# Performance work log

Hardware: AMD Instinct MI355X
Metric: run time of the kernel (lower is better)

## Reference

```python
import jax, jax.numpy as jnp
import numpy as np

B, C, H, W = 2, 512, 32, 32
HEADS = 8      # attention heads
GROUPS = 8     # offset groups (defaults to heads)
DH = 64        # dim_head
DF = 4         # downsample_factor
OFF_SCALE = 4.0
EPS = 1e-5


def _bn(t, gamma, beta):
    # eval-mode BatchNorm2d with running_mean=0, running_var=1
    s = gamma / jnp.sqrt(1.0 + EPS)
    return t * s[None, :, None, None] + beta[None, :, None, None]


def _gconv1x1(t, w):
    # grouped 1x1 conv (bias-free); w: (GROUPS, out_per_group, in_per_group)
    b, c, h, ww = t.shape
    o = jnp.einsum('bgci,goc->bgoi', t.reshape(b, GROUPS, c // GROUPS, h * ww), w)
    return o.reshape(b, GROUPS * w.shape[1], h, ww)


def _grid_sample(img, grid):
    # F.grid_sample: bilinear, padding_mode='zeros', align_corners=False
    # img: (N,Ci,Hi,Wi); grid: (N,Hg,Wg,2), grid[...,0]=x, grid[...,1]=y in [-1,1]
    N, Ci, Hi, Wi = img.shape
    gx = (grid[..., 0] + 1.0) * (Wi / 2.0) - 0.5
    gy = (grid[..., 1] + 1.0) * (Hi / 2.0) - 0.5
    x0 = jnp.floor(gx)
    y0 = jnp.floor(gy)
    wx = gx - x0
    wy = gy - y0

    def gather(im, ix, iy):
        valid = (ix >= 0) & (ix < Wi) & (iy >= 0) & (iy < Hi)
        ixc = jnp.clip(ix, 0, Wi - 1).astype(jnp.int32)
        iyc = jnp.clip(iy, 0, Hi - 1).astype(jnp.int32)
        return im[:, iyc, ixc] * valid[None].astype(im.dtype)

    def sample_one(im, x0, y0, wx, wy):
        v00 = gather(im, x0, y0)
        v01 = gather(im, x0 + 1, y0)
        v10 = gather(im, x0, y0 + 1)
        v11 = gather(im, x0 + 1, y0 + 1)
        wx = wx[None]
        wy = wy[None]
        return (v00 * (1 - wx) * (1 - wy) + v01 * wx * (1 - wy)
                + v10 * (1 - wx) * wy + v11 * wx * wy)

    return jax.vmap(sample_one)(img, x0, y0, wx, wy)


def _forward(x, bn1_g, bn1_b, bn2_g, bn2_b, qw, kw, vw, out_w, out_b,
             off_dw_w, off_dw_b, off_pw_w,
             cpb_w1, cpb_b1, cpb_w2, cpb_b2, cpb_w3, cpb_b3,
             mlp_w1, mlp_b1, mlp_w2, mlp_b2):
    b = x.shape[0]
    xn = _bn(x, bn1_g, bn1_b)
    # ---- deformable attention ----
    q = _gconv1x1(xn, qw)                                   # (b, 512, H, W)
    qg = q.reshape(b * GROUPS, DH, H, W)
    # to_offsets: depthwise conv k=6, s=4, p=1 -> GELU -> 1x1(64->2) -> tanh * offset_scale
    off = jax.lax.conv_general_dilated(
        qg, off_dw_w, (DF, DF), ((1, 1), (1, 1)),
        dimension_numbers=('NCHW', 'OIHW', 'NCHW'), feature_group_count=DH)
    off = jax.nn.gelu(off + off_dw_b[None, :, None, None], approximate=False)
    off = jnp.tanh(jnp.einsum('bchw,oc->bohw', off, off_pw_w)) * OFF_SCALE   # (b*G, 2, Hd, Wd)
    Hd, Wd = off.shape[-2], off.shape[-1]
    gy, gx = jnp.meshgrid(jnp.arange(Hd, dtype=x.dtype), jnp.arange(Wd, dtype=x.dtype), indexing='ij')
    vx = gx[None] + off[:, 0]
    vy = gy[None] + off[:, 1]
    # normalize_grid (lucidrains): first comp by (Hd-1), second by (Wd-1)
    nx = 2.0 * vx / max(Hd - 1, 1) - 1.0
    ny = 2.0 * vy / max(Wd - 1, 1) - 1.0
    vgrid_scaled = jnp.stack((nx, ny), axis=-1)             # (b*G, Hd, Wd, 2)
    kv = _grid_sample(xn.reshape(b * GROUPS, DH, H, W), vgrid_scaled)
    kv = kv.reshape(b, GROUPS * DH, Hd, Wd)
    k = _gconv1x1(kv, kw)
    v = _gconv1x1(kv, vw)
    scale = DH ** -0.5
    qh = q.reshape(b, HEADS, DH, H * W).transpose(0, 1, 3, 2) * scale    # (b,h,i,d)
    kh = k.reshape(b, HEADS, DH, Hd * Wd).transpose(0, 1, 3, 2)          # (b,h,j,d)
    vh = v.reshape(b, HEADS, DH, Hd * Wd).transpose(0, 1, 3, 2)
    # continuous relative position bias (CPB)
    qgy, qgx = jnp.meshgrid(jnp.arange(H, dtype=x.dtype), jnp.arange(W, dtype=x.dtype), indexing='ij')
    grid_q = jnp.stack((2.0 * qgx / max(H - 1, 1) - 1.0,
                        2.0 * qgy / max(W - 1, 1) - 1.0), axis=-1).reshape(1, H * W, 2)
    grid_kv = vgrid_scaled.reshape(b * GROUPS, Hd * Wd, 2)
    pos = grid_q[:, :, None, :] - grid_kv[:, None, :, :]    # (b*G, i, j, 2)
    bias = jnp.sign(pos) * jnp.log1p(jnp.abs(pos))
    bias = jax.nn.relu(bias @ cpb_w1 + cpb_b1)
    bias = jax.nn.relu(bias @ cpb_w2 + cpb_b2)
    bias = (bias @ cpb_w3 + cpb_b3).reshape(b, GROUPS, H * W, Hd * Wd)   # heads//groups == 1
    sim = jnp.einsum('bhid,bhjd->bhij', qh, kh) + bias
    attn = jax.nn.softmax(sim, axis=-1)
    out = jnp.einsum('bhij,bhjd->bhid', attn, vh)
    out = out.transpose(0, 1, 3, 2).reshape(b, HEADS * DH, H, W)
    out = jnp.einsum('bchw,oc->bohw', out, out_w) + out_b[None, :, None, None]
    x = x + out
    # ---- conv1x1 MLP ----
    xn2 = _bn(x, bn2_g, bn2_b)
    h1 = jax.nn.gelu(jnp.einsum('bchw,oc->bohw', xn2, mlp_w1) + mlp_b1[None, :, None, None],
                     approximate=False)
    return x + jnp.einsum('bchw,oc->bohw', h1, mlp_w2) + mlp_b2[None, :, None, None]


def setup_inputs():
    ks = jax.random.split(jax.random.key(0), 16)
    w = lambda k, shape: jax.random.normal(k, shape, dtype=jnp.float32) * 0.02
    return {
        'x': jax.random.normal(ks[0], (B, C, H, W), dtype=jnp.float32),
        'bn1_g': jnp.ones((C,), jnp.float32),
        'bn1_b': jnp.zeros((C,), jnp.float32),
        'bn2_g': jnp.ones((C,), jnp.float32),
        'bn2_b': jnp.zeros((C,), jnp.float32),
        'qw': w(ks[1], (GROUPS, DH, C // GROUPS)),
        'kw': w(ks[2], (GROUPS, DH, C // GROUPS)),
        'vw': w(ks[3], (GROUPS, DH, C // GROUPS)),
        'out_w': w(ks[4], (C, HEADS * DH)),
        'out_b': jnp.zeros((C,), jnp.float32),
        'off_dw_w': w(ks[5], (DH, 1, 6, 6)),
        'off_dw_b': jnp.zeros((DH,), jnp.float32),
        'off_pw_w': w(ks[6], (2, DH)),
        'cpb_w1': w(ks[7], (2, 128)),
        'cpb_b1': jnp.zeros((128,), jnp.float32),
        'cpb_w2': w(ks[8], (128, 128)),
        'cpb_b2': jnp.zeros((128,), jnp.float32),
        'cpb_w3': w(ks[9], (128, 1)),
        'cpb_b3': jnp.zeros((1,), jnp.float32),
        'mlp_w1': w(ks[10], (4 * C, C)),
        'mlp_b1': jnp.zeros((4 * C,), jnp.float32),
        'mlp_w2': w(ks[11], (C, 4 * C)),
        'mlp_b2': jnp.zeros((C,), jnp.float32),
    }


def reference(x, bn1_g, bn1_b, bn2_g, bn2_b, qw, kw, vw, out_w, out_b,
              off_dw_w, off_dw_b, off_pw_w,
              cpb_w1, cpb_b1, cpb_w2, cpb_b2, cpb_w3, cpb_b3,
              mlp_w1, mlp_b1, mlp_w2, mlp_b2):
    return _forward(x, bn1_g, bn1_b, bn2_g, bn2_b, qw, kw, vw, out_w, out_b,
                    off_dw_w, off_dw_b, off_pw_w,
                    cpb_w1, cpb_b1, cpb_w2, cpb_b2, cpb_w3, cpb_b3,
                    mlp_w1, mlp_b1, mlp_w2, mlp_b2)
```

## Files before the change

### kernel.cpp

```cpp
#include <hip/hip_runtime.h>
#include <hip/hip_bf16.h>
#include <math.h>

#define BB 2
#define CC 512
#define HH 32
#define WW 32
#define HWP 1024
#define GG 8
#define DH 64
#define HD 8
#define WD 8
#define JJ 64
#define BG 16
#define EPS 1e-5f

typedef __attribute__((ext_vector_type(8))) short short8;
typedef __attribute__((ext_vector_type(4))) short s16x4;
typedef __attribute__((ext_vector_type(4))) float f32x4;
typedef __attribute__((ext_vector_type(4))) unsigned short u16x4;
typedef __attribute__((ext_vector_type(4))) unsigned int u32x4;

static __device__ __forceinline__ short f2bf(float x) {
    unsigned u = __builtin_bit_cast(unsigned, x);
    u += 0x7FFFu + ((u >> 16) & 1u);
    return (short)(u >> 16);
}

__global__ void k_wpack(const float* __restrict__ qw, const float* __restrict__ ow,
                        const float* __restrict__ w1, const float* __restrict__ w2,
                        const float* __restrict__ cw2, unsigned short* __restrict__ wp,
                        unsigned short* __restrict__ w2p) {
    int idx = blockIdx.x * 256 + threadIdx.x;
    if (idx < 2392064) {
        float v;
        if (idx < 32768) v = qw[idx];
        else if (idx < 294912) v = ow[idx - 32768];
        else if (idx < 1343488) v = w1[idx - 294912];
        else v = w2[idx - 1343488];
        wp[idx] = (unsigned short)f2bf(v);
    } else if (idx < 2408448) {
        int i2 = idx - 2392064;
        int k = i2 >> 7, n = i2 & 127;
        int dest = ((((n >> 4) * 4 + (k >> 5)) * 64) + (((k >> 3) & 3) * 16) + (n & 15)) * 8 + (k & 7);
        w2p[dest] = (unsigned short)f2bf(cw2[i2]);
    }
}

__global__ __launch_bounds__(256) void k_qgemm(
    const float* __restrict__ x, const float* __restrict__ g1,
    const float* __restrict__ b1, const unsigned short* __restrict__ qwp,
    float* __restrict__ q) {
    __shared__ __align__(16) short As[64][72];
    __shared__ __align__(16) short Bs[64][72];
    int blk = blockIdx.x;
    int bg = blk >> 4, nt = blk & 15;
    int b = bg >> 3, g = bg & 7;
    int i0 = nt * 64;
    int tid = threadIdx.x, lane = tid & 63, wv = tid >> 6;
    int wm = (wv >> 1) * 32, wn = (wv & 1) * 32;
    int l15 = lane & 15, quad = lane >> 4;
    const float invs = 1.0f / sqrtf(1.0f + EPS);
    {
        int c4 = (tid & 15) * 4;
        int ob = tid >> 4;
#pragma unroll
        for (int p = 0; p < 4; p++) {
            int o = ob + p * 16;
            u16x4 v = *(const u16x4*)(qwp + (size_t)(g * 64 + o) * 64 + c4);
            *(u16x4*)&As[o][c4] = v;
        }
    }
    {
        int i4 = (tid & 15) * 4;
        int cb = tid >> 4;
#pragma unroll
        for (int p = 0; p < 4; p++) {
            int c = cb + p * 16;
            f32x4 v = *(const f32x4*)(x + (size_t)(b * CC + g * 64 + c) * HWP + i0 + i4);
            float sc = g1[g * 64 + c] * invs;
            float sh = b1[g * 64 + c];
            Bs[i4 + 0][c] = f2bf(fmaf(v.x, sc, sh));
            Bs[i4 + 1][c] = f2bf(fmaf(v.y, sc, sh));
            Bs[i4 + 2][c] = f2bf(fmaf(v.z, sc, sh));
            Bs[i4 + 3][c] = f2bf(fmaf(v.w, sc, sh));
        }
    }
    __syncthreads();
    f32x4 acc[2][2];
#pragma unroll
    for (int a = 0; a < 2; a++)
#pragma unroll
        for (int c = 0; c < 2; c++) acc[a][c] = (f32x4){0.f, 0.f, 0.f, 0.f};
#pragma unroll
    for (int ks = 0; ks < 2; ks++) {
        short8 af0 = *(const short8*)&As[wm + l15][ks * 32 + quad * 8];
        short8 af1 = *(const short8*)&As[wm + 16 + l15][ks * 32 + quad * 8];
        short8 bf0 = *(const short8*)&Bs[wn + l15][ks * 32 + quad * 8];
        short8 bf1 = *(const short8*)&Bs[wn + 16 + l15][ks * 32 + quad * 8];
        acc[0][0] = __builtin_amdgcn_mfma_f32_16x16x32_bf16(af0, bf0, acc[0][0], 0, 0, 0);
        acc[0][1] = __builtin_amdgcn_mfma_f32_16x16x32_bf16(af0, bf1, acc[0][1], 0, 0, 0);
        acc[1][0] = __builtin_amdgcn_mfma_f32_16x16x32_bf16(af1, bf0, acc[1][0], 0, 0, 0);
        acc[1][1] = __builtin_amdgcn_mfma_f32_16x16x32_bf16(af1, bf1, acc[1][1], 0, 0, 0);
    }
#pragma unroll
    for (int im = 0; im < 2; im++)
#pragma unroll
        for (int r = 0; r < 4; r++) {
            int m = wm + im * 16 + quad * 4 + r;
#pragma unroll
            for (int in_ = 0; in_ < 2; in_++) {
                int n = wn + in_ * 16 + l15;
                q[(size_t)(bg * 64 + m) * HWP + i0 + n] = acc[im][in_][r];
            }
        }
}

__global__ void k_off(const float* __restrict__ q, const float* __restrict__ dww,
                      const float* __restrict__ dwb, const float* __restrict__ pw,
                      float* __restrict__ vgrid) {
    int blk = blockIdx.x;
    int bg = blk >> 6;
    int hd = (blk >> 3) & 7;
    int wd = blk & 7;
    int ch = threadIdx.x;
    const float* qch = q + (size_t)(bg * 64 + ch) * HWP;
    float acc = 0.f;
#pragma unroll
    for (int kh = 0; kh < 6; kh++) {
        int hin = hd * 4 - 1 + kh;
        if (hin < 0 || hin >= HH) continue;
#pragma unroll
        for (int kw_ = 0; kw_ < 6; kw_++) {
            int win = wd * 4 - 1 + kw_;
            if (win < 0 || win >= WW) continue;
            acc = fmaf(qch[hin * WW + win], dww[ch * 36 + kh * 6 + kw_], acc);
        }
    }
    acc += dwb[ch];
    float ge = 0.5f * acc * (1.0f + erff(acc * 0.7071067811865475f));
    float p0 = ge * pw[ch];
    float p1 = ge * pw[64 + ch];
#pragma unroll
    for (int off = 32; off; off >>= 1) {
        p0 += __shfl_xor(p0, off);
        p1 += __shfl_xor(p1, off);
    }
    if (ch == 0) {
        float off0 = tanhf(p0) * 4.0f;
        float off1 = tanhf(p1) * 4.0f;
        float vx = (float)wd + off0;
        float vy = (float)hd + off1;
        float nx = 2.0f * vx / 7.0f - 1.0f;
        float ny = 2.0f * vy / 7.0f - 1.0f;
        vgrid[blk * 2] = nx;
        vgrid[blk * 2 + 1] = ny;
    }
}

__global__ __launch_bounds__(64) void k_skv(
    const float* __restrict__ x, const float* __restrict__ g1,
    const float* __restrict__ b1, const float* __restrict__ vgrid,
    const float* __restrict__ kw, const float* __restrict__ vw,
    float* __restrict__ kk, float* __restrict__ vv) {
    __shared__ float sm[64];
    int blk = blockIdx.x;
    int bg = blk >> 6, j = blk & 63;
    int g = bg & 7, b = bg >> 3;
    int t = threadIdx.x;
    const float invs = 1.0f / sqrtf(1.0f + EPS);
    {
        int cg = g * 64 + t;
        float s = g1[cg] * invs;
        float bv = b1[cg];
        float nx = vgrid[blk * 2];
        float ny = vgrid[blk * 2 + 1];
        float gx = (nx + 1.0f) * 16.0f - 0.5f;
        float gy = (ny + 1.0f) * 16.0f - 0.5f;
        float x0f = floorf(gx), y0f = floorf(gy);
        float wx = gx - x0f, wy = gy - y0f;
        int x0 = (int)x0f, y0 = (int)y0f;
        const float* im = x + (size_t)(b * CC + cg) * HWP;
        float sx = 0.f, sw = 0.f;
        float w00 = (1 - wx) * (1 - wy), w01 = wx * (1 - wy);
        float w10 = (1 - wx) * wy, w11 = wx * wy;
        if (x0 >= 0 && x0 < WW && y0 >= 0 && y0 < HH)                 { sx += w00 * im[y0 * WW + x0];           sw += w00; }
        if (x0 + 1 >= 0 && x0 + 1 < WW && y0 >= 0 && y0 < HH)         { sx += w01 * im[y0 * WW + x0 + 1];       sw += w01; }
        if (x0 >= 0 && x0 < WW && y0 + 1 >= 0 && y0 + 1 < HH)         { sx += w10 * im[(y0 + 1) * WW + x0];     sw += w10; }
        if (x0 + 1 >= 0 && x0 + 1 < WW && y0 + 1 >= 0 && y0 + 1 < HH) { sx += w11 * im[(y0 + 1) * WW + x0 + 1]; sw += w11; }
        sm[t] = s * sx + bv * sw;
    }
    __syncthreads();
    const float* kwr = kw + (size_t)(g * 64 + t) * 64;
    const float* vwr = vw + (size_t)(g * 64 + t) * 64;
    float ak = 0.f, av = 0.f;
#pragma unroll
    for (int c = 0; c < 64; c++) {
        float tv = sm[c];
        ak = fmaf(tv, kwr[c], ak);
        av = fmaf(tv, vwr[c], av);
    }
    kk[(size_t)bg * 4096 + j * 64 + t] = ak;
    vv[(size_t)bg * 4096 + j * 64 + t] = av;
}

__global__ __launch_bounds__(256) void k_cpb(
    const float* __restrict__ vgrid, const unsigned short* __restrict__ w2p,
    const float* __restrict__ w1, const float* __restrict__ b1,
    const float* __restrict__ b2, const float* __restrict__ w3,
    const float* __restrict__ b3, float* __restrict__ bias) {
    __shared__ __align__(16) short w2fs[16384];
    __shared__ __align__(16) float coef[640];
    int tid = threadIdx.x;
    {
        const u32x4* src = (const u32x4*)w2p;
        u32x4* dst = (u32x4*)w2fs;
        for (int c = tid; c < 2048; c += 256) dst[c] = src[c];
    }
    if (tid < 256) coef[tid] = w1[tid];
    else if (tid < 384) coef[tid] = b1[tid - 256];
    else if (tid < 512) coef[tid] = b2[tid - 384];
    if (tid >= 128 && tid < 256) coef[512 + tid - 128] = w3[tid - 128];
    float bias3 = b3[0];
    __syncthreads();

    int lane = tid & 63;
    int wv = tid >> 6;
    int l15 = lane & 15;
    int quad = lane >> 4;

#pragma unroll 1
    for (int it = 0; it < 4; it++) {
        int p = (blockIdx.x * 4 + it) * 4 + wv;
        int bg = p >> 11;
        int i = (p >> 1) & 1023;
        int jbase = (p & 1) * 32;
        int hi = i >> 5, wi = i & 31;
        float qx = 2.0f * (float)wi / 31.0f - 1.0f;
        float qy = 2.0f * (float)hi / 31.0f - 1.0f;

        int jA = jbase + l15;
        float gkxA = vgrid[(bg * 64 + jA) * 2];
        float gkyA = vgrid[(bg * 64 + jA) * 2 + 1];
        float gkxB = vgrid[(bg * 64 + jA + 16) * 2];
        float gkyB = vgrid[(bg * 64 + jA + 16) * 2 + 1];
        float p0 = qx - gkxA, p1 = qy - gkyA;
        float s0a = copysignf(log1pf(fabsf(p0)), p0);
        float s1a = copysignf(log1pf(fabsf(p1)), p1);
        p0 = qx - gkxB; p1 = qy - gkyB;
        float s0b = copysignf(log1pf(fabsf(p0)), p0);
        float s1b = copysignf(log1pf(fabsf(p1)), p1);

        short8 hA[4], hB[4];
#pragma unroll
        for (int kc = 0; kc < 4; kc++) {
            f32x4 cu0 = *(const f32x4*)&coef[kc * 32 + quad * 8];
            f32x4 cu1 = *(const f32x4*)&coef[kc * 32 + quad * 8 + 4];
            f32x4 cv0 = *(const f32x4*)&coef[128 + kc * 32 + quad * 8];
            f32x4 cv1 = *(const f32x4*)&coef[128 + kc * 32 + quad * 8 + 4];
            f32x4 cb0 = *(const f32x4*)&coef[256 + kc * 32 + quad * 8];
            f32x4 cb1 = *(const f32x4*)&coef[256 + kc * 32 + quad * 8 + 4];
            u32x4 pa, pb;
#pragma unroll
            for (int j2 = 0; j2 < 4; j2++) {
                int e0 = 2 * j2, e1 = 2 * j2 + 1;
                float u0 = (e0 < 4) ? cu0[e0] : cu1[e0 - 4];
                float u1 = (e1 < 4) ? cu0[e1] : cu1[e1 - 4];
                float v0 = (e0 < 4) ? cv0[e0] : cv1[e0 - 4];
                float v1 = (e1 < 4) ? cv0[e1] : cv1[e1 - 4];
                float c0 = (e0 < 4) ? cb0[e0] : cb1[e0 - 4];
                float c1 = (e1 < 4) ? cb0[e1] : cb1[e1 - 4];
                unsigned a0 = __builtin_bit_cast(unsigned,
                    fmaxf(fmaf(s0a, u0, fmaf(s1a, v0, c0)), 0.f)) + 0x8000u;
                unsigned a1 = __builtin_bit_cast(unsigned,
                    fmaxf(fmaf(s0a, u1, fmaf(s1a, v1, c1)), 0.f)) + 0x8000u;
                pa[j2] = __builtin_amdgcn_perm(a1, a0, 0x07060302);
                unsigned b0 = __builtin_bit_cast(unsigned,
                    fmaxf(fmaf(s0b, u0, fmaf(s1b, v0, c0)), 0.f)) + 0x8000u;
                unsigned b1_ = __builtin_bit_cast(unsigned,
                    fmaxf(fmaf(s0b, u1, fmaf(s1b, v1, c1)), 0.f)) + 0x8000u;
                pb[j2] = __builtin_amdgcn_perm(b1_, b0, 0x07060302);
            }
            hA[kc] = __builtin_bit_cast(short8, pa);
            hB[kc] = __builtin_bit_cast(short8, pb);
        }

        float psumA = 0.f, psumB = 0.f;
#pragma unroll 2
        for (int nt = 0; nt < 8; nt++) {
            f32x4 accA = (f32x4){0.f, 0.f, 0.f, 0.f};
            f32x4 accB = (f32x4){0.f, 0.f, 0.f, 0.f};
#pragma unroll
            for (int kc = 0; kc < 4; kc++) {
                short8 af = *(const short8*)(w2fs + (((nt * 4 + kc) * 64) + lane) * 8);
                accA = __builtin_amdgcn_mfma_f32_16x16x32_bf16(af, hA[kc], accA, 0, 0, 0);
                accB = __builtin_amdgcn_mfma_f32_16x16x32_bf16(af, hB[kc], accB, 0, 0, 0);
            }
            f32x4 b2q = *(const f32x4*)&coef[384 + nt * 16 + quad * 4];
            f32x4 w3q = *(const f32x4*)&coef[512 + nt * 16 + quad * 4];
#pragma unroll
            for (int r = 0; r < 4; r++) {
                psumA = fmaf(fmaxf(accA[r] + b2q[r], 0.f), w3q[r], psumA);
                psumB = fmaf(fmaxf(accB[r] + b2q[r], 0.f), w3q[r], psumB);
            }
        }
        psumA += __shfl_xor(psumA, 16);
        psumA += __shfl_xor(psumA, 32);
        psumB += __shfl_xor(psumB, 16);
        psumB += __shfl_xor(psumB, 32);
        if (quad == 0) {
            bias[(size_t)(p * 2 + 0) * 16 + l15] = psumA + bias3;
            bias[(size_t)(p * 2 + 1) * 16 + l15] = psumB + bias3;
        }
    }
}

__global__ __launch_bounds__(256) void k_attn(
    const float* __restrict__ q, const float* __restrict__ kk,
    const float* __restrict__ vv, const float* __restrict__ bias,
    unsigned short* __restrict__ ao) {
    __shared__ __align__(16) short Ks[64][72];
    __shared__ __align__(16) short Vt[64][72];
    __shared__ __align__(16) short Qs[64][72];
    __shared__ __align__(16) short Ps[4][16][72];
    int blk = blockIdx.x;
    int bg = blk >> 4;
    int chunk = blk & 15;
    int i0 = chunk * 64;
    int b = bg >> 3, g = bg & 7;
    int tid = threadIdx.x, lane = tid & 63, wv = tid >> 6;
    int l15 = lane & 15, quad = lane >> 4;

    const float* kbase = kk + (size_t)bg * 4096;
    const float* vbase = vv + (size_t)bg * 4096;
#pragma unroll
    for (int it = 0; it < 4; it++) {
        int e4 = it * 1024 + tid * 4;
        int j = e4 >> 6, d = e4 & 63;
        f32x4 k4 = *(const f32x4*)(kbase + e4);
        s16x4 s = {f2bf(k4.x), f2bf(k4.y), f2bf(k4.z), f2bf(k4.w)};
        *(s16x4*)&Ks[j][d] = s;
        f32x4 v4 = *(const f32x4*)(vbase + e4);
        Vt[d + 0][j] = f2bf(v4.x);
        Vt[d + 1][j] = f2bf(v4.y);
        Vt[d + 2][j] = f2bf(v4.z);
        Vt[d + 3][j] = f2bf(v4.w);
    }
    const float* qbase = q + (size_t)(b * CC + g * 64) * HWP + i0;
#pragma unroll
    for (int it = 0; it < 4; it++) {
        int e4 = it * 1024 + tid * 4;
        int d = e4 >> 6, i = e4 & 63;
        f32x4 q4 = *(const f32x4*)(qbase + (size_t)d * HWP + i);
        Qs[i + 0][d] = f2bf(q4.x * 0.125f);
        Qs[i + 1][d] = f2bf(q4.y * 0.125f);
        Qs[i + 2][d] = f2bf(q4.z * 0.125f);
        Qs[i + 3][d] = f2bf(q4.w * 0.125f);
    }
    __syncthreads();

    int iw = wv * 16;
    f32x4 Sacc[4];
#pragma unroll
    for (int nt = 0; nt < 4; nt++) Sacc[nt] = (f32x4){0.f, 0.f, 0.f, 0.f};
#pragma unroll
    for (int ks = 0; ks < 2; ks++) {
        short8 aq = *(const short8*)&Qs[iw + l15][quad * 8 + ks * 32];
#pragma unroll
        for (int nt = 0; nt < 4; nt++) {
            short8 bk = *(const short8*)&Ks[nt * 16 + l15][quad * 8 + ks * 32];
            Sacc[nt] = __builtin_amdgcn_mfma_f32_16x16x32_bf16(aq, bk, Sacc[nt], 0, 0, 0);
        }
    }
    const float* bp = bias + ((size_t)bg * 1024 + i0 + iw + quad * 4) * 64 + l15;
    float Sv[4][4];
#pragma unroll
    for (int nt = 0; nt < 4; nt++)
#pragma unroll
        for (int r = 0; r < 4; r++)
            Sv[nt][r] = Sacc[nt][r] + bp[r * 64 + nt * 16];
#pragma unroll
    for (int r = 0; r < 4; r++) {
        float m = fmaxf(fmaxf(Sv[0][r], Sv[1][r]), fmaxf(Sv[2][r], Sv[3][r]));
        m = fmaxf(m, __shfl_xor(m, 1));
        m = fmaxf(m, __shfl_xor(m, 2));
        m = fmaxf(m, __shfl_xor(m, 4));
        m = fmaxf(m, __shfl_xor(m, 8));
        float l = 0.f;
#pragma unroll
        for (int nt = 0; nt < 4; nt++) { Sv[nt][r] = expf(Sv[nt][r] - m); l += Sv[nt][r]; }
        l += __shfl_xor(l, 1);
        l += __shfl_xor(l, 2);
        l += __shfl_xor(l, 4);
        l += __shfl_xor(l, 8);
        float inv = 1.0f / l;
#pragma unroll
        for (int nt = 0; nt < 4; nt++)
            Ps[wv][quad * 4 + r][nt * 16 + l15] = f2bf(Sv[nt][r] * inv);
    }
    f32x4 Oacc[4];
#pragma unroll
    for (int nt = 0; nt < 4; nt++) Oacc[nt] = (f32x4){0.f, 0.f, 0.f, 0.f};
#pragma unroll
    for (int ks = 0; ks < 2; ks++) {
        short8 ap = *(const short8*)&Ps[wv][l15][quad * 8 + ks * 32];
#pragma unroll
        for (int nt = 0; nt < 4; nt++) {
            short8 bv = *(const short8*)&Vt[nt * 16 + l15][quad * 8 + ks * 32];
            Oacc[nt] = __builtin_amdgcn_mfma_f32_16x16x32_bf16(ap, bv, Oacc[nt], 0, 0, 0);
        }
    }
    __syncthreads();
#pragma unroll
    for (int nt = 0; nt < 4; nt++) {
        s16x4 o4 = {f2bf(Oacc[nt][0]), f2bf(Oacc[nt][1]), f2bf(Oacc[nt][2]), f2bf(Oacc[nt][3])};
        *(s16x4*)&Qs[nt * 16 + l15][iw + quad * 4] = o4;
    }
    __syncthreads();
    {
        int d = tid >> 2;
        int ic = (tid & 3) * 16;
        short8 a = *(const short8*)&Qs[d][ic];
        short8 c = *(const short8*)&Qs[d][ic + 8];
        unsigned short* dst = ao + (size_t)(b * CC + g * 64 + d) * HWP + i0 + ic;
        *(short8*)dst = a;
        *(short8*)(dst + 8) = c;
    }
}

template<int EPI, int KD, int MT, bool BBF>
__global__ __launch_bounds__(256) void k_gemm(
    const unsigned short* __restrict__ A, const void* __restrict__ Bp,
    const float* __restrict__ resid, const float* __restrict__ bias,
    void* __restrict__ outp, unsigned short* __restrict__ out2,
    const float* __restrict__ bns, const float* __restrict__ bnb) {
    constexpr int MM = MT * 64;
    __shared__ __align__(16) short As[64][72];
    __shared__ __align__(16) short Bs[64][72];
    int tid = threadIdx.x;
    int blk = blockIdx.x;
    int mt = blk & (MT - 1);
    int nb = blk / MT;
    int bb = nb >> 4, nt = nb & 15;
    int m0 = mt * 64, i0 = nt * 64;
    int lane = tid & 63, wv = tid >> 6;
    int wm = (wv >> 1) * 32, wn = (wv & 1) * 32;
    int l15 = lane & 15, quad = lane >> 4;
    const unsigned short* Af = A + (size_t)m0 * KD;
    const float* Bf = (const float*)Bp;
    const unsigned short* Bh = (const unsigned short*)Bp;
    const float invs = 1.0f / sqrtf(1.0f + EPS);

    f32x4 acc[2][2];
#pragma unroll
    for (int a = 0; a < 2; a++)
#pragma unroll
        for (int c = 0; c < 2; c++) acc[a][c] = (f32x4){0.f, 0.f, 0.f, 0.f};

    for (int k0 = 0; k0 < KD; k0 += 64) {
        __syncthreads();
        {
            int kk4 = (tid & 15) * 4;
            int myb = tid >> 4;
#pragma unroll
            for (int p = 0; p < 4; p++) {
                int my = myb + p * 16;
                u16x4 v = *(const u16x4*)(Af + (size_t)my * KD + k0 + kk4);
                *(u16x4*)&As[my][kk4] = v;
            }
        }
        {
            int i4 = (tid & 15) * 4;
            int kyb = tid >> 4;
#pragma unroll
            for (int p = 0; p < 4; p++) {
                int ky = kyb + p * 16;
                size_t goff = (size_t)bb * KD * HWP + (size_t)(k0 + ky) * HWP + i0 + i4;
                if (BBF) {
                    u16x4 v = *(const u16x4*)(Bh + goff);
                    Bs[i4 + 0][ky] = (short)v.x;
                    Bs[i4 + 1][ky] = (short)v.y;
                    Bs[i4 + 2][ky] = (short)v.z;
                    Bs[i4 + 3][ky] = (short)v.w;
                } else {
                    f32x4 v = *(const f32x4*)(Bf + goff);
                    Bs[i4 + 0][ky] = f2bf(v.x);
                    Bs[i4 + 1][ky] = f2bf(v.y);
                    Bs[i4 + 2][ky] = f2bf(v.z);
                    Bs[i4 + 3][ky] = f2bf(v.w);
                }
            }
        }
        __syncthreads();
#pragma unroll
        for (int ks = 0; ks < 2; ks++) {
            short8 af0 = *(const short8*)&As[wm + l15][ks * 32 + quad * 8];
            short8 af1 = *(const short8*)&As[wm + 16 + l15][ks * 32 + quad * 8];
            short8 bf0 = *(const short8*)&Bs[wn + l15][ks * 32 + quad * 8];
            short8 bf1 = *(const short8*)&Bs[wn + 16 + l15][ks * 32 + quad * 8];
            acc[0][0] = __builtin_amdgcn_mfma_f32_16x16x32_bf16(af0, bf0, acc[0][0], 0, 0, 0);
            acc[0][1] = __builtin_amdgcn_mfma_f32_16x16x32_bf16(af0, bf1, acc[0][1], 0, 0, 0);
            acc[1][0] = __builtin_amdgcn_mfma_f32_16x16x32_bf16(af1, bf0, acc[1][0], 0, 0, 0);
            acc[1][1] = __builtin_amdgcn_mfma_f32_16x16x32_bf16(af1, bf1, acc[1][1], 0, 0, 0);
        }
    }

    float* outF = (float*)outp;
    unsigned short* outH = (unsigned short*)outp;
#pragma unroll
    for (int im = 0; im < 2; im++) {
#pragma unroll
        for (int r = 0; r < 4; r++) {
            int m = m0 + wm + im * 16 + quad * 4 + r;
            float bv = bias[m];
#pragma unroll
            for (int in_ = 0; in_ < 2; in_++) {
                int n = i0 + wn + in_ * 16 + l15;
                size_t idx = ((size_t)bb * MM + m) * HWP + n;
                float v = acc[im][in_][r] + bv;
                if constexpr (EPI == 1) {
                    float ge = 0.5f * v * (1.0f + erff(v * 0.7071067811865475f));
                    outH[idx] = (unsigned short)f2bf(ge);
                } else if constexpr (EPI == 3) {
                    float vr = v + resid[idx];
                    outF[idx] = vr;
                    out2[idx] = (unsigned short)f2bf(fmaf(vr, bns[m] * invs, bnb[m]));
                } else {
                    outF[idx] = v + resid[idx];
                }
            }
        }
    }
}

extern "C" void kernel_launch(void* const* d_in, const int* in_sizes, int n_in,
                              void* d_out, int out_size, void* d_ws, size_t ws_size,
                              hipStream_t stream) {
    const float* x      = (const float*)d_in[0];
    const float* bn1_g  = (const float*)d_in[1];
    const float* bn1_b  = (const float*)d_in[2];
    const float* bn2_g  = (const float*)d_in[3];
    const float* bn2_b  = (const float*)d_in[4];
    const float* qw     = (const float*)d_in[5];
    const float* kw     = (const float*)d_in[6];
    const float* vw     = (const float*)d_in[7];
    const float* out_w  = (const float*)d_in[8];
    const float* out_b  = (const float*)d_in[9];
    const float* off_dw_w = (const float*)d_in[10];
    const float* off_dw_b = (const float*)d_in[11];
    const float* off_pw_w = (const float*)d_in[12];
    const float* cpb_w1 = (const float*)d_in[13];
    const float* cpb_b1 = (const float*)d_in[14];
    const float* cpb_w2 = (const float*)d_in[15];
    const float* cpb_b2 = (const float*)d_in[16];
    const float* cpb_w3 = (const float*)d_in[17];
    const float* cpb_b3 = (const float*)d_in[18];
    const float* mlp_w1 = (const float*)d_in[19];
    const float* mlp_b1 = (const float*)d_in[20];
    const float* mlp_w2 = (const float*)d_in[21];
    const float* mlp_b2 = (const float*)d_in[22];

    float* ws = (float*)d_ws;
    float* q     = ws + 1048576;
    float* vgrid = ws + 2097152;
    float* kk    = ws + 2164736;
    float* vv    = ws + 2230272;
    unsigned short* w2p = (unsigned short*)(ws + 2295808);
    unsigned short* ao  = (unsigned short*)(ws + 2312192);
    unsigned short* xn2 = (unsigned short*)(ws + 2836480);
    float* xo    = ws + 3360768;
    float* h1of  = ws + 4409344;
    float* biasb = h1of;
    unsigned short* h1o = (unsigned short*)h1of;
    unsigned short* wp  = (unsigned short*)(ws + 6506496);
    unsigned short* qwp  = wp;
    unsigned short* owp  = wp + 32768;
    unsigned short* w1p  = wp + 294912;
    unsigned short* w2mp = wp + 1343488;

    hipLaunchKernelGGL(k_wpack, dim3(9408), dim3(256), 0, stream,
                       qw, out_w, mlp_w1, mlp_w2, cpb_w2, wp, w2p);
    hipLaunchKernelGGL(k_qgemm, dim3(256), dim3(256), 0, stream, x, bn1_g, bn1_b, qwp, q);
    hipLaunchKernelGGL(k_off, dim3(1024), dim3(64), 0, stream, q, off_dw_w, off_dw_b, off_pw_w, vgrid);
    hipLaunchKernelGGL(k_skv, dim3(1024), dim3(64), 0, stream, x, bn1_g, bn1_b, vgrid, kw, vw, kk, vv);
    hipLaunchKernelGGL(k_cpb, dim3(2048), dim3(256), 0, stream,
                       vgrid, w2p, cpb_w1, cpb_b1, cpb_b2, cpb_w3, cpb_b3, biasb);
    hipLaunchKernelGGL(k_attn, dim3(256), dim3(256), 0, stream, q, kk, vv, biasb, ao);
    k_gemm<3, 512, 8, true><<<dim3(256), dim3(256), 0, stream>>>(
        owp, ao, x, out_b, xo, xn2, bn2_g, bn2_b);
    k_gemm<1, 512, 32, true><<<dim3(1024), dim3(256), 0, stream>>>(
        w1p, xn2, nullptr, mlp_b1, h1o, nullptr, nullptr, nullptr);
    k_gemm<2, 2048, 8, true><<<dim3(256), dim3(256), 0, stream>>>(
        w2mp, h1o, xo, mlp_b2, d_out, nullptr, nullptr, nullptr);
}
```

Measured before the change: 276.1 us.

## Store q as transposed bf16, fuse offset and sampling kernels, deepen GEMM K-tile

The q projection is now written as bf16 in a position-major (transposed) layout through a shared-memory transpose. This halves q traffic and lets the attention kernel copy Q tiles directly, with the 1/8 scale folded into the score FMA. The offset kernel and the sampled K/V kernel are merged into one launch that computes the grid point in-register, removing a kernel and the vgrid round trip. The generic GEMM gets a configurable K-tile, set to 128, to halve its barrier count per K step at the cost of more shared memory. Quantising q to bf16 before the depthwise offset conv adds a small accuracy risk.

```diff
diff --git a/kernel.cpp b/kernel.cpp
--- a/kernel.cpp
+++ b/kernel.cpp
@@ -25,6 +25,9 @@
     unsigned u = __builtin_bit_cast(unsigned, x);
     u += 0x7FFFu + ((u >> 16) & 1u);
     return (short)(u >> 16);
+}
+static __device__ __forceinline__ float bf2f(unsigned short h) {
+    return __builtin_bit_cast(float, (unsigned)h << 16);
 }
 
 __global__ void k_wpack(const float* __restrict__ qw, const float* __restrict__ ow,
@@ -50,7 +53,7 @@
 __global__ __launch_bounds__(256) void k_qgemm(
     const float* __restrict__ x, const float* __restrict__ g1,
     const float* __restrict__ b1, const unsigned short* __restrict__ qwp,
-    float* __restrict__ q) {
+    unsigned short* __restrict__ qt) {
     __shared__ __align__(16) short As[64][72];
     __shared__ __align__(16) short Bs[64][72];
     int blk = blockIdx.x;
@@ -103,6 +106,7 @@
         acc[1][0] = __builtin_amdgcn_mfma_f32_16x16x32_bf16(af1, bf0, acc[1][0], 0, 0, 0);
         acc[1][1] = __builtin_amdgcn_mfma_f32_16x16x32_bf16(af1, bf1, acc[1][1], 0, 0, 0);
     }
+    __syncthreads();
 #pragma unroll
     for (int im = 0; im < 2; im++)
 #pragma unroll
@@ -111,20 +115,36 @@
 #pragma unroll
             for (int in_ = 0; in_ < 2; in_++) {
                 int n = wn + in_ * 16 + l15;
-                q[(size_t)(bg * 64 + m) * HWP + i0 + n] = acc[im][in_][r];
-            }
-        }
-}
-
-__global__ void k_off(const float* __restrict__ q, const float* __restrict__ dww,
-                      const float* __restrict__ dwb, const float* __restrict__ pw,
-                      float* __restrict__ vgrid) {
+                As[n][m] = f2bf(acc[im][in_][r]);
+            }
+        }
+    __syncthreads();
+    {
+        int n = tid >> 2;
+        int c0 = (tid & 3) * 16;
+        short8 a = *(const short8*)&As[n][c0];
+        short8 c = *(const short8*)&As[n][c0 + 8];
+        unsigned short* dst = qt + ((size_t)bg * 1024 + i0 + n) * 64 + c0;
+        *(short8*)dst = a;
+        *(short8*)(dst + 8) = c;
+    }
+}
+
+__global__ __launch_bounds__(64) void k_offskv(
+    const unsigned short* __restrict__ qt, const float* __restrict__ dww,
+    const float* __restrict__ dwb, const float* __restrict__ pw,
+    const float* __restrict__ x, const float* __restrict__ g1,
+    const float* __restrict__ b1, const float* __restrict__ kw,
+    const float* __restrict__ vw, float* __restrict__ vgrid,
+    float* __restrict__ kk, float* __restrict__ vv) {
+    __shared__ float sm[64];
     int blk = blockIdx.x;
     int bg = blk >> 6;
     int hd = (blk >> 3) & 7;
     int wd = blk & 7;
+    int g = bg & 7, b = bg >> 3;
     int ch = threadIdx.x;
-    const float* qch = q + (size_t)(bg * 64 + ch) * HWP;
+    const unsigned short* qb = qt + (size_t)bg * 65536;
     float acc = 0.f;
 #pragma unroll
     for (int kh = 0; kh < 6; kh++) {
@@ -134,7 +154,7 @@
         for (int kw_ = 0; kw_ < 6; kw_++) {
             int win = wd * 4 - 1 + kw_;
             if (win < 0 || win >= WW) continue;
-            acc = fmaf(qch[hin * WW + win], dww[ch * 36 + kh * 6 + kw_], acc);
+            acc = fmaf(bf2f(qb[(hin * WW + win) * 64 + ch]), dww[ch * 36 + kh * 6 + kw_], acc);
         }
     }
     acc += dwb[ch];
@@ -146,35 +166,17 @@
         p0 += __shfl_xor(p0, off);
         p1 += __shfl_xor(p1, off);
     }
+    float nx = 2.0f * ((float)wd + tanhf(p0) * 4.0f) / 7.0f - 1.0f;
+    float ny = 2.0f * ((float)hd + tanhf(p1) * 4.0f) / 7.0f - 1.0f;
     if (ch == 0) {
-        float off0 = tanhf(p0) * 4.0f;
-        float off1 = tanhf(p1) * 4.0f;
-        float vx = (float)wd + off0;
-        float vy = (float)hd + off1;
-        float nx = 2.0f * vx / 7.0f - 1.0f;
-        float ny = 2.0f * vy / 7.0f - 1.0f;
         vgrid[blk * 2] = nx;
         vgrid[blk * 2 + 1] = ny;
     }
-}
-
-__global__ __launch_bounds__(64) void k_skv(
-    const float* __restrict__ x, const float* __restrict__ g1,
-    const float* __restrict__ b1, const float* __restrict__ vgrid,
-    const float* __restrict__ kw, const float* __restrict__ vw,
-    float* __restrict__ kk, float* __restrict__ vv) {
-    __shared__ float sm[64];
-    int blk = blockIdx.x;
-    int bg = blk >> 6, j = blk & 63;
-    int g = bg & 7, b = bg >> 3;
-    int t = threadIdx.x;
-    const float invs = 1.0f / sqrtf(1.0f + EPS);
-    {
-        int cg = g * 64 + t;
+    {
+        int cg = g * 64 + ch;
+        const float invs = 1.0f / sqrtf(1.0f + EPS);
         float s = g1[cg] * invs;
         float bv = b1[cg];
-        float nx = vgrid[blk * 2];
-        float ny = vgrid[blk * 2 + 1];
         float gx = (nx + 1.0f) * 16.0f - 0.5f;
         float gy = (ny + 1.0f) * 16.0f - 0.5f;
         float x0f = floorf(gx), y0f = floorf(gy);
@@ -188,11 +190,12 @@
         if (x0 + 1 >= 0 && x0 + 1 < WW && y0 >= 0 && y0 < HH)         { sx += w01 * im[y0 * WW + x0 + 1];       sw += w01; }
         if (x0 >= 0 && x0 < WW && y0 + 1 >= 0 && y0 + 1 < HH)         { sx += w10 * im[(y0 + 1) * WW + x0];     sw += w10; }
         if (x0 + 1 >= 0 && x0 + 1 < WW && y0 + 1 >= 0 && y0 + 1 < HH) { sx += w11 * im[(y0 + 1) * WW + x0 + 1]; sw += w11; }
-        sm[t] = s * sx + bv * sw;
-    }
-    __syncthreads();
-    const float* kwr = kw + (size_t)(g * 64 + t) * 64;
-    const float* vwr = vw + (size_t)(g * 64 + t) * 64;
+        sm[ch] = s * sx + bv * sw;
+    }
+    __syncthreads();
+    int j = blk & 63;
+    const float* kwr = kw + (size_t)(g * 64 + ch) * 64;
+    const float* vwr = vw + (size_t)(g * 64 + ch) * 64;
     float ak = 0.f, av = 0.f;
 #pragma unroll
     for (int c = 0; c < 64; c++) {
@@ -200,8 +203,8 @@
         ak = fmaf(tv, kwr[c], ak);
         av = fmaf(tv, vwr[c], av);
     }
-    kk[(size_t)bg * 4096 + j * 64 + t] = ak;
-    vv[(size_t)bg * 4096 + j * 64 + t] = av;
+    kk[(size_t)bg * 4096 + j * 64 + ch] = ak;
+    vv[(size_t)bg * 4096 + j * 64 + ch] = av;
 }
 
 __global__ __launch_bounds__(256) void k_cpb(
@@ -316,7 +319,7 @@
 }
 
 __global__ __launch_bounds__(256) void k_attn(
-    const float* __restrict__ q, const float* __restrict__ kk,
+    const unsigned short* __restrict__ qt, const float* __restrict__ kk,
     const float* __restrict__ vv, const float* __restrict__ bias,
     unsigned short* __restrict__ ao) {
     __shared__ __align__(16) short Ks[64][72];
@@ -346,16 +349,15 @@
         Vt[d + 2][j] = f2bf(v4.z);
         Vt[d + 3][j] = f2bf(v4.w);
     }
-    const float* qbase = q + (size_t)(b * CC + g * 64) * HWP + i0;
-#pragma unroll
-    for (int it = 0; it < 4; it++) {
-        int e4 = it * 1024 + tid * 4;
-        int d = e4 >> 6, i = e4 & 63;
-        f32x4 q4 = *(const f32x4*)(qbase + (size_t)d * HWP + i);
-        Qs[i + 0][d] = f2bf(q4.x * 0.125f);
-        Qs[i + 1][d] = f2bf(q4.y * 0.125f);
-        Qs[i + 2][d] = f2bf(q4.z * 0.125f);
-        Qs[i + 3][d] = f2bf(q4.w * 0.125f);
+    {
+        const unsigned short* qtb = qt + ((size_t)bg * 1024 + i0) * 64;
+#pragma unroll
+        for (int it = 0; it < 4; it++) {
+            int e4 = it * 1024 + tid * 4;
+            int i = e4 >> 6, d = e4 & 63;
+            u16x4 v = *(const u16x4*)(qtb + e4);
+            *(u16x4*)&Qs[i][d] = v;
+        }
     }
     __syncthreads();
 
@@ -378,7 +380,7 @@
     for (int nt = 0; nt < 4; nt++)
 #pragma unroll
         for (int r = 0; r < 4; r++)
-            Sv[nt][r] = Sacc[nt][r] + bp[r * 64 + nt * 16];
+            Sv[nt][r] = fmaf(Sacc[nt][r], 0.125f, bp[r * 64 + nt * 16]);
 #pragma unroll
     for (int r = 0; r < 4; r++) {
         float m = fmaxf(fmaxf(Sv[0][r], Sv[1][r]), fmaxf(Sv[2][r], Sv[3][r]));
@@ -428,15 +430,15 @@
     }
 }
 
-template<int EPI, int KD, int MT, bool BBF>
+template<int EPI, int KD, int BK, int MT>
 __global__ __launch_bounds__(256) void k_gemm(
-    const unsigned short* __restrict__ A, const void* __restrict__ Bp,
+    const unsigned short* __restrict__ A, const unsigned short* __restrict__ Bh,
     const float* __restrict__ resid, const float* __restrict__ bias,
     void* __restrict__ outp, unsigned short* __restrict__ out2,
     const float* __restrict__ bns, const float* __restrict__ bnb) {
     constexpr int MM = MT * 64;
-    __shared__ __align__(16) short As[64][72];
-    __shared__ __align__(16) short Bs[64][72];
+    __shared__ __align__(16) short As[64][BK + 8];
+    __shared__ __align__(16) short Bs[64][BK + 8];
     int tid = threadIdx.x;
     int blk = blockIdx.x;
     int mt = blk & (MT - 1);
@@ -447,8 +449,6 @@
     int wm = (wv >> 1) * 32, wn = (wv & 1) * 32;
     int l15 = lane & 15, quad = lane >> 4;
     const unsigned short* Af = A + (size_t)m0 * KD;
-    const float* Bf = (const float*)Bp;
-    const unsigned short* Bh = (const unsigned short*)Bp;
     const float invs = 1.0f / sqrtf(1.0f + EPS);
 
     f32x4 acc[2][2];
@@ -457,14 +457,15 @@
 #pragma unroll
         for (int c = 0; c < 2; c++) acc[a][c] = (f32x4){0.f, 0.f, 0.f, 0.f};
 
-    for (int k0 = 0; k0 < KD; k0 += 64) {
+    for (int k0 = 0; k0 < KD; k0 += BK) {
         __syncthreads();
         {
-            int kk4 = (tid & 15) * 4;
-            int myb = tid >> 4;
-#pragma unroll
-            for (int p = 0; p < 4; p++) {
-                int my = myb + p * 16;
+            int kk4 = (tid & (BK / 4 - 1)) * 4;
+            int myb = tid / (BK / 4);
+            constexpr int RP = 256 / (BK / 4);
+#pragma unroll
+            for (int p = 0; p < 64 / RP; p++) {
+                int my = myb + p * RP;
                 u16x4 v = *(const u16x4*)(Af + (size_t)my * KD + k0 + kk4);
                 *(u16x4*)&As[my][kk4] = v;
             }
@@ -473,27 +474,19 @@
             int i4 = (tid & 15) * 4;
             int kyb = tid >> 4;
 #pragma unroll
-            for (int p = 0; p < 4; p++) {
+            for (int p = 0; p < BK / 16; p++) {
                 int ky = kyb + p * 16;
                 size_t goff = (size_t)bb * KD * HWP + (size_t)(k0 + ky) * HWP + i0 + i4;
-                if (BBF) {
-                    u16x4 v = *(const u16x4*)(Bh + goff);
-                    Bs[i4 + 0][ky] = (short)v.x;
-                    Bs[i4 + 1][ky] = (short)v.y;
-                    Bs[i4 + 2][ky] = (short)v.z;
-                    Bs[i4 + 3][ky] = (short)v.w;
-                } else {
-                    f32x4 v = *(const f32x4*)(Bf + goff);
-                    Bs[i4 + 0][ky] = f2bf(v.x);
-                    Bs[i4 + 1][ky] = f2bf(v.y);
-                    Bs[i4 + 2][ky] = f2bf(v.z);
-                    Bs[i4 + 3][ky] = f2bf(v.w);
-                }
+                u16x4 v = *(const u16x4*)(Bh + goff);
+                Bs[i4 + 0][ky] = (short)v.x;
+                Bs[i4 + 1][ky] = (short)v.y;
+                Bs[i4 + 2][ky] = (short)v.z;
+                Bs[i4 + 3][ky] = (short)v.w;
             }
         }
         __syncthreads();
 #pragma unroll
-        for (int ks = 0; ks < 2; ks++) {
+        for (int ks = 0; ks < BK / 32; ks++) {
             short8 af0 = *(const short8*)&As[wm + l15][ks * 32 + quad * 8];
             short8 af1 = *(const short8*)&As[wm + 16 + l15][ks * 32 + quad * 8];
             short8 bf0 = *(const short8*)&Bs[wn + l15][ks * 32 + quad * 8];
@@ -561,7 +554,7 @@
     const float* mlp_b2 = (const float*)d_in[22];
 
     float* ws = (float*)d_ws;
-    float* q     = ws + 1048576;
+    unsigned short* qt = (unsigned short*)(ws + 1048576);
     float* vgrid = ws + 2097152;
     float* kk    = ws + 2164736;
     float* vv    = ws + 2230272;
@@ -580,16 +573,17 @@
 
     hipLaunchKernelGGL(k_wpack, dim3(9408), dim3(256), 0, stream,
                        qw, out_w, mlp_w1, mlp_w2, cpb_w2, wp, w2p);
-    hipLaunchKernelGGL(k_qgemm, dim3(256), dim3(256), 0, stream, x, bn1_g, bn1_b, qwp, q);
-    hipLaunchKernelGGL(k_off, dim3(1024), dim3(64), 0, stream, q, off_dw_w, off_dw_b, off_pw_w, vgrid);
-    hipLaunchKernelGGL(k_skv, dim3(1024), dim3(64), 0, stream, x, bn1_g, bn1_b, vgrid, kw, vw, kk, vv);
+    hipLaunchKernelGGL(k_qgemm, dim3(256), dim3(256), 0, stream, x, bn1_g, bn1_b, qwp, qt);
+    hipLaunchKernelGGL(k_offskv, dim3(1024), dim3(64), 0, stream,
+                       qt, off_dw_w, off_dw_b, off_pw_w, x, bn1_g, bn1_b, kw, vw,
+                       vgrid, kk, vv);
     hipLaunchKernelGGL(k_cpb, dim3(2048), dim3(256), 0, stream,
                        vgrid, w2p, cpb_w1, cpb_b1, cpb_b2, cpb_w3, cpb_b3, biasb);
-    hipLaunchKernelGGL(k_attn, dim3(256), dim3(256), 0, stream, q, kk, vv, biasb, ao);
-    k_gemm<3, 512, 8, true><<<dim3(256), dim3(256), 0, stream>>>(
+    hipLaunchKernelGGL(k_attn, dim3(256), dim3(256), 0, stream, qt, kk, vv, biasb, ao);
+    k_gemm<3, 512, 128, 8><<<dim3(256), dim3(256), 0, stream>>>(
         owp, ao, x, out_b, xo, xn2, bn2_g, bn2_b);
-    k_gemm<1, 512, 32, true><<<dim3(1024), dim3(256), 0, stream>>>(
+    k_gemm<1, 512, 128, 32><<<dim3(1024), dim3(256), 0, stream>>>(
         w1p, xn2, nullptr, mlp_b1, h1o, nullptr, nullptr, nullptr);
-    k_gemm<2, 2048, 8, true><<<dim3(256), dim3(256), 0, stream>>>(
+    k_gemm<2, 2048, 128, 8><<<dim3(256), dim3(256), 0, stream>>>(
         w2mp, h1o, xo, mlp_b2, d_out, nullptr, nullptr, nullptr);
 }
```

After: 262.0 us. -5.1%, faster.
